# Kernel tuning notes

Hardware: AMD Instinct MI355X
Metric: run time of the kernel (lower is better)

## Reference

```python
import jax, jax.numpy as jnp
import numpy as np

N_BITS = 4
GROUP_SIZE = 128
CLIP_RATIO = 1.0  # no clipping when == 1.0
EPS = 1e-5


def setup_inputs() -> dict:
    key = jax.random.key(0)
    k1, k2 = jax.random.split(key)
    B, S, C = 4, 4096, 4096
    x = jax.random.normal(k1, (B, S, C), dtype=jnp.float32)
    perm = jax.random.permutation(k2, C).astype(jnp.int32)
    inv = jnp.argsort(perm).astype(jnp.int32)
    return {"x": x, "perm_indices": perm, "inverse_perm_indices": inv}


def _quantize_groupwise(w):
    """Asymmetric int quant/dequant, quant_method='max', per flat group of GROUP_SIZE."""
    saved_shape = w.shape
    g = w.reshape(-1, GROUP_SIZE)  # [num_groups, group_size]
    q_max = 2 ** N_BITS - 1  # asym: q_min = 0
    w_max = jnp.max(g, axis=-1, keepdims=True)
    w_min = jnp.min(g, axis=-1, keepdims=True)
    scales = jnp.clip(w_max - w_min, EPS, None) / q_max
    base = jnp.clip(jnp.round(-w_min / scales), 0, q_max)
    q = (jnp.clip(jnp.round(g / scales) + base, 0, q_max) - base) * scales
    return q.reshape(saved_shape)


def reference(x, perm_indices, inverse_perm_indices):
    # cluster-based channel permutation -> group-wise quant/dequant -> inverse permutation
    x_perm = jnp.take(x, perm_indices, axis=-1)
    x_q = _quantize_groupwise(x_perm)
    return jnp.take(x_q, inverse_perm_indices, axis=-1)
```

## Files before the change

kernel.cpp:

```cpp
#include <hip/hip_runtime.h>
#include <stdint.h>


constexpr int C     = 4096;
constexpr int GS    = 128;
constexpr int NG    = C / GS;
constexpr int BLOCK = 512;
constexpr int WAVES = BLOCK / 64;
constexpr int GPW   = NG / WAVES;
constexpr int EPL   = GS / 16;
constexpr int VECS  = C / 4 / BLOCK;

typedef const __attribute__((address_space(1))) uint32_t glb_u32;
typedef __attribute__((address_space(3))) uint32_t lds_u32;

__device__ __forceinline__ void stage_row(const float* __restrict__ src,
                                          float* dst, int wave, int lane) {
    #pragma unroll
    for (int i = 0; i < 2; ++i) {
        const float* g = src + i * 2048 + wave * 256 + lane * 4;
        float*       l = dst + i * 2048 + wave * 256;
        __builtin_amdgcn_global_load_lds((glb_u32*)(uintptr_t)g,
                                         (lds_u32*)(uintptr_t)l, 16, 0, 0);
    }
}

__global__ __launch_bounds__(BLOCK, 8) void tpq_kernel(
    const float* __restrict__ x,
    const int*   __restrict__ gat,
    const int*   __restrict__ asn,
    float*       __restrict__ out,
    int rows)
{
    __shared__ float  rowbuf[2][C];
    __shared__ float2 sb[2][NG];

    const int tid  = threadIdx.x;
    const int wave = tid >> 6;
    const int lane = tid & 63;
    const int sub  = lane >> 4;
    const int sl   = lane & 15;
    const int g    = wave * GPW + sub;

    int pidx[EPL];
    {
        const int4* g4 = reinterpret_cast<const int4*>(gat + g * GS + sl * EPL);
        const int4 a = g4[0], b = g4[1];
        pidx[0] = a.x; pidx[1] = a.y; pidx[2] = a.z; pidx[3] = a.w;
        pidx[4] = b.x; pidx[5] = b.y; pidx[6] = b.z; pidx[7] = b.w;
    }
    uint32_t gpack[VECS];
    #pragma unroll
    for (int i = 0; i < VECS; ++i) {
        const int4 a = reinterpret_cast<const int4*>(asn)[tid + i * BLOCK];
        gpack[i] = (uint32_t)(a.x >> 7)        | ((uint32_t)(a.y >> 7) << 8)
                 | ((uint32_t)(a.z >> 7) << 16) | ((uint32_t)(a.w >> 7) << 24);
    }

    int r = blockIdx.x;
    stage_row(x + (size_t)r * C, rowbuf[0], wave, lane);
    __syncthreads();
    int cur = 0;

    while (true) {
        const int  rn = r + gridDim.x;
        const bool hn = rn < rows;
        if (hn) stage_row(x + (size_t)rn * C, rowbuf[cur ^ 1], wave, lane);

        const float* rc = rowbuf[cur];
        float v0 = rc[pidx[0]], v1 = rc[pidx[1]], v2 = rc[pidx[2]], v3 = rc[pidx[3]];
        float v4 = rc[pidx[4]], v5 = rc[pidx[5]], v6 = rc[pidx[6]], v7 = rc[pidx[7]];
        float mx = fmaxf(fmaxf(fmaxf(v0, v1), fmaxf(v2, v3)),
                         fmaxf(fmaxf(v4, v5), fmaxf(v6, v7)));
        float mn = fminf(fminf(fminf(v0, v1), fminf(v2, v3)),
                         fminf(fminf(v4, v5), fminf(v6, v7)));
        #pragma unroll
        for (int off = 8; off; off >>= 1) {
            mx = fmaxf(mx, __shfl_xor(mx, off));
            mn = fminf(mn, __shfl_xor(mn, off));
        }
        if (sl == 0) {
            const float s = fmaxf(mx - mn, 1e-5f) * (1.0f / 15.0f);
            const float b = fminf(fmaxf(rintf(-mn / s), 0.0f), 15.0f);
            sb[cur][g] = make_float2(s, b);
        }

        asm volatile("s_waitcnt lgkmcnt(0)\n\ts_barrier" ::: "memory");

        const float4*  rc4 = reinterpret_cast<const float4*>(rc);
        const float2*  sbc = sb[cur];
        float4*        or4 = reinterpret_cast<float4*>(out + (size_t)r * C);
        #pragma unroll
        for (int i = 0; i < VECS; ++i) {
            const float4   v  = rc4[tid + i * BLOCK];
            const uint32_t gp = gpack[i];
            float4 o;
            { const float2 p = sbc[gp & 31u];
              o.x = (fminf(fmaxf(rintf(v.x / p.x) + p.y, 0.0f), 15.0f) - p.y) * p.x; }
            { const float2 p = sbc[(gp >> 8) & 31u];
              o.y = (fminf(fmaxf(rintf(v.y / p.x) + p.y, 0.0f), 15.0f) - p.y) * p.x; }
            { const float2 p = sbc[(gp >> 16) & 31u];
              o.z = (fminf(fmaxf(rintf(v.z / p.x) + p.y, 0.0f), 15.0f) - p.y) * p.x; }
            { const float2 p = sbc[(gp >> 24) & 31u];
              o.w = (fminf(fmaxf(rintf(v.w / p.x) + p.y, 0.0f), 15.0f) - p.y) * p.x; }
            or4[tid + i * BLOCK] = o;
        }

        if (!hn) break;
        r = rn;
        cur ^= 1;
        __syncthreads();
    }
}

extern "C" void kernel_launch(void* const* d_in, const int* in_sizes, int n_in,
                              void* d_out, int out_size, void* d_ws, size_t ws_size,
                              hipStream_t stream) {
    const float* x   = (const float*)d_in[0];
    const int*   gat = (const int*)d_in[1];
    const int*   asn = (const int*)d_in[2];
    float* out = (float*)d_out;

    const int rows = in_sizes[0] / C;
    const int nblk = rows < 2048 ? rows : 2048;

    tpq_kernel<<<nblk, BLOCK, 0, stream>>>(x, gat, asn, out, rows);
}
```

Baseline: 104.7 us.

## Software-pipeline stats and quantization across rows with register prefetch and DPP reductions

Replaces the async global-to-LDS row staging with register prefetch of the next row. The loop is restructured so each iteration computes group min/max stats for the current row while quantizing the previous row, cutting one barrier per iteration. Shuffle-based reductions are replaced with DPP row moves. This raises register pressure (prefetched float4 array) and adds a skewed pipeline with an epilogue.

```diff
diff --git a/kernel.cpp b/kernel.cpp
--- a/kernel.cpp
+++ b/kernel.cpp
@@ -6,22 +6,35 @@
 constexpr int GS    = 128;
 constexpr int NG    = C / GS;
 constexpr int BLOCK = 512;
-constexpr int WAVES = BLOCK / 64;
-constexpr int GPW   = NG / WAVES;
-constexpr int EPL   = GS / 16;
+constexpr int GPW   = 4;
 constexpr int VECS  = C / 4 / BLOCK;
 
-typedef const __attribute__((address_space(1))) uint32_t glb_u32;
-typedef __attribute__((address_space(3))) uint32_t lds_u32;
+template<int CTRL>
+__device__ __forceinline__ float dpp_mov(float x) {
+    return __int_as_float(__builtin_amdgcn_update_dpp(
+        0, __float_as_int(x), CTRL, 0xF, 0xF, true));
+}
 
-__device__ __forceinline__ void stage_row(const float* __restrict__ src,
-                                          float* dst, int wave, int lane) {
+__device__ __forceinline__ void quant_row(
+    const float* rcbase, const float2* sbc, float* outrow,
+    int tid, const uint32_t* gpack)
+{
+    const float4* rc4 = reinterpret_cast<const float4*>(rcbase);
+    float4*       or4 = reinterpret_cast<float4*>(outrow);
     #pragma unroll
-    for (int i = 0; i < 2; ++i) {
-        const float* g = src + i * 2048 + wave * 256 + lane * 4;
-        float*       l = dst + i * 2048 + wave * 256;
-        __builtin_amdgcn_global_load_lds((glb_u32*)(uintptr_t)g,
-                                         (lds_u32*)(uintptr_t)l, 16, 0, 0);
+    for (int i = 0; i < VECS; ++i) {
+        const float4   v  = rc4[tid + i * BLOCK];
+        const uint32_t gp = gpack[i];
+        float4 o;
+        { const float2 p = sbc[gp & 31u];
+          o.x = (fminf(fmaxf(rintf(v.x / p.x) + p.y, 0.0f), 15.0f) - p.y) * p.x; }
+        { const float2 p = sbc[(gp >> 8) & 31u];
+          o.y = (fminf(fmaxf(rintf(v.y / p.x) + p.y, 0.0f), 15.0f) - p.y) * p.x; }
+        { const float2 p = sbc[(gp >> 16) & 31u];
+          o.z = (fminf(fmaxf(rintf(v.z / p.x) + p.y, 0.0f), 15.0f) - p.y) * p.x; }
+        { const float2 p = sbc[(gp >> 24) & 31u];
+          o.w = (fminf(fmaxf(rintf(v.w / p.x) + p.y, 0.0f), 15.0f) - p.y) * p.x; }
+        or4[tid + i * BLOCK] = o;
     }
 }
 
@@ -42,9 +55,9 @@
     const int sl   = lane & 15;
     const int g    = wave * GPW + sub;
 
-    int pidx[EPL];
+    int pidx[8];
     {
-        const int4* g4 = reinterpret_cast<const int4*>(gat + g * GS + sl * EPL);
+        const int4* g4 = reinterpret_cast<const int4*>(gat + g * GS + sl * 8);
         const int4 a = g4[0], b = g4[1];
         pidx[0] = a.x; pidx[1] = a.y; pidx[2] = a.z; pidx[3] = a.w;
         pidx[4] = b.x; pidx[5] = b.y; pidx[6] = b.z; pidx[7] = b.w;
@@ -58,59 +71,70 @@
     }
 
     int r = blockIdx.x;
-    stage_row(x + (size_t)r * C, rowbuf[0], wave, lane);
-    __syncthreads();
-    int cur = 0;
+    const int stride = gridDim.x;
 
+    {
+        const float4* x4  = reinterpret_cast<const float4*>(x + (size_t)r * C);
+        float4*       rw4 = reinterpret_cast<float4*>(rowbuf[0]);
+        #pragma unroll
+        for (int i = 0; i < VECS; ++i) rw4[tid + i * BLOCK] = x4[tid + i * BLOCK];
+        __syncthreads();
+    }
+
+    int cur = 0, rp = -1;
     while (true) {
-        const int  rn = r + gridDim.x;
+        const int  rn = r + stride;
         const bool hn = rn < rows;
-        if (hn) stage_row(x + (size_t)rn * C, rowbuf[cur ^ 1], wave, lane);
 
-        const float* rc = rowbuf[cur];
-        float v0 = rc[pidx[0]], v1 = rc[pidx[1]], v2 = rc[pidx[2]], v3 = rc[pidx[3]];
-        float v4 = rc[pidx[4]], v5 = rc[pidx[5]], v6 = rc[pidx[6]], v7 = rc[pidx[7]];
-        float mx = fmaxf(fmaxf(fmaxf(v0, v1), fmaxf(v2, v3)),
-                         fmaxf(fmaxf(v4, v5), fmaxf(v6, v7)));
-        float mn = fminf(fminf(fminf(v0, v1), fminf(v2, v3)),
-                         fminf(fminf(v4, v5), fminf(v6, v7)));
-        #pragma unroll
-        for (int off = 8; off; off >>= 1) {
-            mx = fmaxf(mx, __shfl_xor(mx, off));
-            mn = fminf(mn, __shfl_xor(mn, off));
-        }
-        if (sl == 0) {
-            const float s = fmaxf(mx - mn, 1e-5f) * (1.0f / 15.0f);
-            const float b = fminf(fmaxf(rintf(-mn / s), 0.0f), 15.0f);
-            sb[cur][g] = make_float2(s, b);
+        float4 vn[VECS];
+        if (hn) {
+            const float4* nx4 = reinterpret_cast<const float4*>(x + (size_t)rn * C);
+            #pragma unroll
+            for (int i = 0; i < VECS; ++i) vn[i] = nx4[tid + i * BLOCK];
         }
 
-        asm volatile("s_waitcnt lgkmcnt(0)\n\ts_barrier" ::: "memory");
-
-        const float4*  rc4 = reinterpret_cast<const float4*>(rc);
-        const float2*  sbc = sb[cur];
-        float4*        or4 = reinterpret_cast<float4*>(out + (size_t)r * C);
-        #pragma unroll
-        for (int i = 0; i < VECS; ++i) {
-            const float4   v  = rc4[tid + i * BLOCK];
-            const uint32_t gp = gpack[i];
-            float4 o;
-            { const float2 p = sbc[gp & 31u];
-              o.x = (fminf(fmaxf(rintf(v.x / p.x) + p.y, 0.0f), 15.0f) - p.y) * p.x; }
-            { const float2 p = sbc[(gp >> 8) & 31u];
-              o.y = (fminf(fmaxf(rintf(v.y / p.x) + p.y, 0.0f), 15.0f) - p.y) * p.x; }
-            { const float2 p = sbc[(gp >> 16) & 31u];
-              o.z = (fminf(fmaxf(rintf(v.z / p.x) + p.y, 0.0f), 15.0f) - p.y) * p.x; }
-            { const float2 p = sbc[(gp >> 24) & 31u];
-              o.w = (fminf(fmaxf(rintf(v.w / p.x) + p.y, 0.0f), 15.0f) - p.y) * p.x; }
-            or4[tid + i * BLOCK] = o;
+        {
+            const float* rc = rowbuf[cur];
+            const float a0 = rc[pidx[0]], a1 = rc[pidx[1]];
+            const float a2 = rc[pidx[2]], a3 = rc[pidx[3]];
+            const float a4 = rc[pidx[4]], a5 = rc[pidx[5]];
+            const float a6 = rc[pidx[6]], a7 = rc[pidx[7]];
+            float mx = fmaxf(fmaxf(fmaxf(a0, a1), fmaxf(a2, a3)),
+                             fmaxf(fmaxf(a4, a5), fmaxf(a6, a7)));
+            float mn = fminf(fminf(fminf(a0, a1), fminf(a2, a3)),
+                             fminf(fminf(a4, a5), fminf(a6, a7)));
+            mx = fmaxf(mx, dpp_mov<0xB1>(mx));
+            mn = fminf(mn, dpp_mov<0xB1>(mn));
+            mx = fmaxf(mx, dpp_mov<0x4E>(mx));
+            mn = fminf(mn, dpp_mov<0x4E>(mn));
+            mx = fmaxf(mx, dpp_mov<0x141>(mx));
+            mn = fminf(mn, dpp_mov<0x141>(mn));
+            mx = fmaxf(mx, dpp_mov<0x140>(mx));
+            mn = fminf(mn, dpp_mov<0x140>(mn));
+            if (sl == 0) {
+                const float s = fmaxf(mx - mn, 1e-5f) * (1.0f / 15.0f);
+                const float b = fminf(fmaxf(rintf(-mn / s), 0.0f), 15.0f);
+                sb[cur][g] = make_float2(s, b);
+            }
         }
 
+        if (rp >= 0)
+            quant_row(rowbuf[cur ^ 1], sb[cur ^ 1], out + (size_t)rp * C,
+                      tid, gpack);
+
         if (!hn) break;
-        r = rn;
-        cur ^= 1;
+
+        {
+            float4* rw4 = reinterpret_cast<float4*>(rowbuf[cur ^ 1]);
+            #pragma unroll
+            for (int i = 0; i < VECS; ++i) rw4[tid + i * BLOCK] = vn[i];
+        }
         __syncthreads();
+        rp = r; r = rn; cur ^= 1;
     }
+
+    __syncthreads();
+    quant_row(rowbuf[cur], sb[cur], out + (size_t)r * C, tid, gpack);
 }
 
 extern "C" void kernel_launch(void* const* d_in, const int* in_sizes, int n_in,
```

Result: slower. 136.0 us (+29.9%).
